# Kernel tuning notes

Hardware: AMD Instinct MI355X
Metric: run time of the kernel (lower is better)

## Reference

```python
import jax, jax.numpy as jnp
import numpy as np

D_MODEL = 1024
N_HEADS = 16
D_HEAD = D_MODEL // N_HEADS


def setup_inputs() -> dict:
    key = jax.random.key(0)
    k_x, k_wqkv, k_bqkv, k_wo, k_bo = jax.random.split(key, 5)
    B, S = 2, 2048
    x = jax.random.normal(k_x, (B, S, D_MODEL), dtype=jnp.float32)
    # torch Linear: y = x @ W.T + b; store W as [out, in] like torch
    bound1 = 1.0 / np.sqrt(D_MODEL)
    W_qkv = jax.random.uniform(k_wqkv, (3 * D_MODEL, D_MODEL), minval=-bound1, maxval=bound1, dtype=jnp.float32)
    b_qkv = jax.random.uniform(k_bqkv, (3 * D_MODEL,), minval=-bound1, maxval=bound1, dtype=jnp.float32)
    W_out = jax.random.uniform(k_wo, (D_MODEL, D_MODEL), minval=-bound1, maxval=bound1, dtype=jnp.float32)
    b_out = jax.random.uniform(k_bo, (D_MODEL,), minval=-bound1, maxval=bound1, dtype=jnp.float32)
    return {"x": x, "W_qkv": W_qkv, "b_qkv": b_qkv, "W_out": W_out, "b_out": b_out}


def reference(x, W_qkv, b_qkv, W_out, b_out):
    B, S, D = x.shape
    qkv = x @ W_qkv.T + b_qkv                       # [B, S, 3D]
    qkv = qkv.reshape(B, S, 3, N_HEADS, D_HEAD)
    qkv = jnp.transpose(qkv, (2, 0, 3, 1, 4))       # [3, B, H, S, Dh]
    q, k, v = qkv[0], qkv[1], qkv[2]
    scores = jnp.einsum('bhqd,bhkd->bhqk', q, k) / np.sqrt(D_HEAD).astype(np.float32)
    causal = jnp.tril(jnp.ones((S, S), dtype=bool))
    scores = jnp.where(causal[None, None], scores, jnp.float32(-jnp.inf))
    attn = jax.nn.softmax(scores, axis=-1)          # dropout p=0 -> identity
    out = jnp.einsum('bhqk,bhkd->bhqd', attn, v)    # [B, H, S, Dh]
    out = jnp.transpose(out, (0, 2, 1, 3)).reshape(B, S, D)
    return out @ W_out.T + b_out
```

## Files before the change

### kernel.cpp

```cpp
#include <hip/hip_runtime.h>
#include <hip/hip_bf16.h>
#include <cstdint>


#define DEV __device__ __forceinline__

#define VT_STRIDE 2048

using bf16x8 = __attribute__((ext_vector_type(8))) short;
using f32x4  = __attribute__((ext_vector_type(4))) float;

DEV unsigned short f2bf(float f) {
  unsigned u = __builtin_bit_cast(unsigned, f);
  u = (u + 0x7fffu + ((u >> 16) & 1u)) >> 16;
  return (unsigned short)u;
}

typedef __attribute__((address_space(1))) unsigned int as1_uint;
typedef __attribute__((address_space(3))) unsigned int as3_uint;

DEV void gload_lds16(const void* g, void* l) {
  __builtin_amdgcn_global_load_lds(
      (as1_uint*)(uintptr_t)g,
      (as3_uint*)(unsigned int)(uintptr_t)l,
      16, 0, 0);
}

#define N4_X  (4096 * 1024 / 4)
#define N4_WQ (3072 * 1024 / 4)
#define N4_WO (1024 * 1024 / 4)
__global__ __launch_bounds__(256) void cvt_all_k(const float* __restrict__ x,
                                                 const float* __restrict__ wq,
                                                 const float* __restrict__ wo,
                                                 unsigned short* __restrict__ xb,
                                                 unsigned short* __restrict__ wqb,
                                                 unsigned short* __restrict__ wob) {
  int i = blockIdx.x * 256 + threadIdx.x;
  const float* in; unsigned short* out;
  if (i < N4_X)                { in = x;  out = xb; }
  else if (i < N4_X + N4_WQ)   { i -= N4_X;  in = wq; out = wqb; }
  else                         { i -= N4_X + N4_WQ; in = wo; out = wob; }
  float4 v = reinterpret_cast<const float4*>(in)[i];
  ushort4 o;
  o.x = f2bf(v.x); o.y = f2bf(v.y); o.z = f2bf(v.z); o.w = f2bf(v.w);
  reinterpret_cast<ushort4*>(out)[i] = o;
}

__global__ __launch_bounds__(256) void transpose_v_k(const unsigned short* __restrict__ V,
                                                     unsigned short* __restrict__ Vt) {
  const int bh = blockIdx.x;
  const int st = blockIdx.y;
  const int tid = threadIdx.x;
  __shared__ unsigned short T[64 * 64];
  const unsigned short* src = V + ((size_t)bh * 2048 + st * 64) * 64;

#pragma unroll
  for (int it = 0; it < 2; ++it) {
    const int c = it * 256 + tid;
    const int L = c * 16;
    const int S = L ^ (((L >> 10) & 7) << 4);
    gload_lds16((const char*)src + S, (char*)T + L);
  }
  __syncthreads();

#pragma unroll
  for (int it = 0; it < 2; ++it) {
    const int c = it * 256 + tid;
    const int d = c >> 3;
    const int s_off = (c & 7) * 8;
    const int xg = (c & 7) << 4;
    bf16x8 pk;
#pragma unroll
    for (int j = 0; j < 8; ++j)
      pk[j] = *(const short*)((const char*)T + (((s_off + j) * 128 + d * 2) ^ xg));
    *(bf16x8*)(Vt + (size_t)(bh * 64 + d) * VT_STRIDE + st * 64 + s_off) = pk;
  }
}

template <int MODE, int N, int K>
__global__ __launch_bounds__(256) void gemm_bt(const unsigned short* __restrict__ A,
                                               const unsigned short* __restrict__ W,
                                               const float* __restrict__ bias,
                                               float* __restrict__ Cout,
                                               unsigned short* __restrict__ Qp,
                                               unsigned short* __restrict__ Kp,
                                               unsigned short* __restrict__ Vp) {
  __shared__ unsigned short As[128 * 64];
  __shared__ unsigned short Bs[128 * 64];
  const int tid = threadIdx.x;
  const int m0 = blockIdx.x * 128;
  const int n0 = blockIdx.y * 128;
  const int w = tid >> 6, lane = tid & 63, g = lane >> 4, lr = lane & 15;
  const int wr = w >> 1, wc = w & 1;
  const int xr = (lr & 7) << 4;

  f32x4 acc[4][4];
#pragma unroll
  for (int i = 0; i < 4; ++i)
#pragma unroll
    for (int j = 0; j < 4; ++j)
#pragma unroll
      for (int r = 0; r < 4; ++r) acc[i][j][r] = 0.f;

  for (int kt = 0; kt < K; kt += 64) {
#pragma unroll
    for (int it = 0; it < 4; ++it) {
      const int c = it * 256 + tid;
      const int row = c >> 3;
      const int colb = ((c & 7) * 16) ^ ((row & 7) << 4);
      gload_lds16((const char*)(A + (size_t)(m0 + row) * K + kt) + colb, (char*)As + c * 16);
      gload_lds16((const char*)(W + (size_t)(n0 + row) * K + kt) + colb, (char*)Bs + c * 16);
    }
    __syncthreads();
#pragma unroll
    for (int ks = 0; ks < 2; ++ks) {
      bf16x8 af[4], bf[4];
#pragma unroll
      for (int mi = 0; mi < 4; ++mi)
        af[mi] = *(const bf16x8*)((const char*)As +
                   ((((wr * 64 + mi * 16 + lr) * 128) + ks * 64 + g * 16) ^ xr));
#pragma unroll
      for (int ni = 0; ni < 4; ++ni)
        bf[ni] = *(const bf16x8*)((const char*)Bs +
                   ((((wc * 64 + ni * 16 + lr) * 128) + ks * 64 + g * 16) ^ xr));
#pragma unroll
      for (int mi = 0; mi < 4; ++mi)
#pragma unroll
        for (int ni = 0; ni < 4; ++ni)
          acc[mi][ni] = __builtin_amdgcn_mfma_f32_16x16x32_bf16(af[mi], bf[ni], acc[mi][ni], 0, 0, 0);
    }
    __syncthreads();
  }

  if (MODE == 0) {
#pragma unroll
    for (int ni = 0; ni < 4; ++ni) {
      const int col = n0 + wc * 64 + ni * 16 + lr;
      const float bv = bias[col];
#pragma unroll
      for (int mi = 0; mi < 4; ++mi)
#pragma unroll
        for (int r = 0; r < 4; ++r) {
          const int row = m0 + wr * 64 + mi * 16 + g * 4 + r;
          Cout[(size_t)row * N + col] = acc[mi][ni][r] + bv;
        }
    }
  } else {
#pragma unroll
    for (int ni = 0; ni < 4; ++ni) {
      const int col = n0 + wc * 64 + ni * 16 + lr;
      const float bv = bias[col];
      const int which = col >> 10;
      const int h = (col >> 6) & 15;
      const int d = col & 63;
      unsigned short* P = which == 0 ? Qp : which == 1 ? Kp : Vp;
#pragma unroll
      for (int mi = 0; mi < 4; ++mi)
#pragma unroll
        for (int r = 0; r < 4; ++r) {
          const int row = m0 + wr * 64 + mi * 16 + g * 4 + r;
          const int b = row >> 11, s = row & 2047;
          P[(((size_t)(b * 16 + h) * 2048 + s) << 6) + d] = f2bf(acc[mi][ni][r] + bv);
        }
    }
  }
}

__global__ __launch_bounds__(256) void attn_fwd(const unsigned short* __restrict__ Q,
                                                const unsigned short* __restrict__ Kg,
                                                const unsigned short* __restrict__ Vt,
                                                unsigned short* __restrict__ AO) {
  const int bh = blockIdx.x;
  const int qb = blockIdx.y;
  const int tid = threadIdx.x;
  const int w = tid >> 6, lane = tid & 63, g = lane >> 4, lr = lane & 15;
  const unsigned short* Qp = Q  + (size_t)bh * 2048 * 64;
  const unsigned short* Kp = Kg + (size_t)bh * 2048 * 64;
  const unsigned short* Vp = Vt + (size_t)bh * 64 * VT_STRIDE;
  const int b = bh >> 4, h = bh & 15;

  __shared__ unsigned short Ks[64 * 64];
  __shared__ unsigned short Vs[64 * 64];
  __shared__ unsigned short Pl[4][16 * 64];

  const float C = 0.1803368801f;
  char* Plw = (char*)Pl[w];
  const int xr = (lr & 7) << 4;

  const int L0 = tid * 16,         L1 = (tid + 256) * 16;
  const int G0 = L0 ^ (((L0 >> 7) & 7) << 4);
  const int G1 = L1 ^ (((L1 >> 7) & 7) << 4);

#pragma unroll
  for (int half = 0; half < 2; ++half) {
    const int qt = half ? (31 - qb) : qb;
    const int nb = qt + 1;
    const int qrow0 = qt * 64 + w * 16;

    bf16x8 aq[2];
#pragma unroll
    for (int ks = 0; ks < 2; ++ks)
      aq[ks] = *(const bf16x8*)(Qp + (size_t)(qrow0 + lr) * 64 + ks * 32 + g * 8);

    f32x4 o[4];
    float lp[4];
#pragma unroll
    for (int db = 0; db < 4; ++db)
#pragma unroll
      for (int r = 0; r < 4; ++r) o[db][r] = 0.f;
#pragma unroll
    for (int r = 0; r < 4; ++r) lp[r] = 0.f;

    for (int t = 0; t < nb; ++t) {
      const int kvb = t * 64;
      gload_lds16((const char*)Kp + (size_t)kvb * 128 + G0, (char*)Ks + L0);
      gload_lds16((const char*)Kp + (size_t)kvb * 128 + G1, (char*)Ks + L1);
      gload_lds16((const char*)Vp + (size_t)(G0 >> 7) * (VT_STRIDE * 2) + (size_t)kvb * 2 + (G0 & 127),
                  (char*)Vs + L0);
      gload_lds16((const char*)Vp + (size_t)(G1 >> 7) * (VT_STRIDE * 2) + (size_t)kvb * 2 + (G1 & 127),
                  (char*)Vs + L1);
      __syncthreads();

      f32x4 sc[4];
#pragma unroll
      for (int f = 0; f < 4; ++f)
#pragma unroll
        for (int r = 0; r < 4; ++r) sc[f][r] = 0.f;
#pragma unroll
      for (int ks = 0; ks < 2; ++ks)
#pragma unroll
        for (int f = 0; f < 4; ++f) {
          bf16x8 bk = *(const bf16x8*)((const char*)Ks + (((f * 16 + lr) * 128 + ks * 64 + g * 16) ^ xr));
          sc[f] = __builtin_amdgcn_mfma_f32_16x16x32_bf16(aq[ks], bk, sc[f], 0, 0, 0);
        }

      if (t == nb - 1) {
#pragma unroll
        for (int r = 0; r < 4; ++r) {
          const int qr = w * 16 + g * 4 + r;
#pragma unroll
          for (int f = 0; f < 4; ++f)
            if (f * 16 + lr > qr) sc[f][r] = -INFINITY;
        }
      }

#pragma unroll
      for (int r = 0; r < 4; ++r) {
        float s0 = exp2f(sc[0][r] * C);
        float s1 = exp2f(sc[1][r] * C);
        float s2 = exp2f(sc[2][r] * C);
        float s3 = exp2f(sc[3][r] * C);
        sc[0][r] = s0; sc[1][r] = s1; sc[2][r] = s2; sc[3][r] = s3;
        lp[r] += (s0 + s1) + (s2 + s3);
      }

#pragma unroll
      for (int r = 0; r < 4; ++r) {
        const int prow = g * 4 + r;
#pragma unroll
        for (int f = 0; f < 4; ++f) {
          const int byte = (prow * 128 + (f * 16 + lr) * 2) ^ ((prow & 7) << 4);
          *(unsigned short*)(Plw + byte) = f2bf(sc[f][r]);
        }
      }
      asm volatile("s_waitcnt lgkmcnt(0)" ::: "memory");
      __builtin_amdgcn_sched_barrier(0);

#pragma unroll
      for (int ks = 0; ks < 2; ++ks) {
        const int pbyte = (lr * 128 + ks * 64 + g * 16) ^ ((lr & 7) << 4);
        bf16x8 pa = *(const bf16x8*)(Plw + pbyte);
#pragma unroll
        for (int db = 0; db < 4; ++db) {
          bf16x8 bv = *(const bf16x8*)((const char*)Vs + (((db * 16 + lr) * 128 + ks * 64 + g * 16) ^ xr));
          o[db] = __builtin_amdgcn_mfma_f32_16x16x32_bf16(pa, bv, o[db], 0, 0, 0);
        }
      }
      __syncthreads();
    }

#pragma unroll
    for (int r = 0; r < 4; ++r) {
      float l = lp[r];
      l += __shfl_xor(l, 1); l += __shfl_xor(l, 2);
      l += __shfl_xor(l, 4); l += __shfl_xor(l, 8);
      lp[r] = 1.0f / l;
    }
#pragma unroll
    for (int r = 0; r < 4; ++r) {
      const int row = qrow0 + g * 4 + r;
#pragma unroll
      for (int db = 0; db < 4; ++db)
        AO[(size_t)(b * 2048 + row) * 1024 + h * 64 + db * 16 + lr] = f2bf(o[db][r] * lp[r]);
    }
  }
}

extern "C" void kernel_launch(void* const* d_in, const int* in_sizes, int n_in,
                              void* d_out, int out_size, void* d_ws, size_t ws_size,
                              hipStream_t stream) {
  const float* x     = (const float*)d_in[0];
  const float* W_qkv = (const float*)d_in[1];
  const float* b_qkv = (const float*)d_in[2];
  const float* W_out = (const float*)d_in[3];
  const float* b_out = (const float*)d_in[4];
  float* out = (float*)d_out;

  char* ws = (char*)d_ws;
  unsigned short* xb  = (unsigned short*)(ws);
  unsigned short* AOb = (unsigned short*)(ws);
  unsigned short* wqb = (unsigned short*)(ws + ((size_t)8 << 20));
  unsigned short* wob = (unsigned short*)(ws + ((size_t)14 << 20));
  unsigned short* Qb  = (unsigned short*)(ws + ((size_t)16 << 20));
  unsigned short* Kb  = (unsigned short*)(ws + ((size_t)24 << 20));
  unsigned short* Vb  = (unsigned short*)(ws + ((size_t)32 << 20));
  unsigned short* Vtb = (unsigned short*)(ws + ((size_t)40 << 20));

  cvt_all_k<<<(N4_X + N4_WQ + N4_WO) / 256, 256, 0, stream>>>(x, W_qkv, W_out, xb, wqb, wob);

  gemm_bt<1, 3072, 1024><<<dim3(32, 24), 256, 0, stream>>>(xb, wqb, b_qkv, nullptr, Qb, Kb, Vb);
  transpose_v_k<<<dim3(32, 32), 256, 0, stream>>>(Vb, Vtb);
  attn_fwd<<<dim3(32, 16), 256, 0, stream>>>(Qb, Kb, Vtb, AOb);
  gemm_bt<0, 1024, 1024><<<dim3(32, 8), 256, 0, stream>>>(AOb, wob, b_out, out, nullptr, nullptr, nullptr);
}
```

Measured before the change: 129.3 us.

## Double-buffer K/V tiles in attention and transpose QK^T MFMA layout

The attention kernel now keeps two LDS buffers for K and V and prefetches the next tile asynchronously while computing the current one, using partial vmcnt waits and raw barriers instead of a full syncthreads per iteration. The QK^T MFMA operands are swapped so each lane holds a score column, which lets P be packed with v_cvt_pk_bf16_f32 and written as 8-byte stores, and reduces the row-sum to two shuffles. s_setprio hints are added around the MFMA blocks. The cost is doubled LDS use for K/V, which may lower occupancy, plus more delicate synchronisation.

```diff
diff --git a/kernel.cpp b/kernel.cpp
--- a/kernel.cpp
+++ b/kernel.cpp
@@ -179,8 +179,8 @@
   const unsigned short* Vp = Vt + (size_t)bh * 64 * VT_STRIDE;
   const int b = bh >> 4, h = bh & 15;
 
-  __shared__ unsigned short Ks[64 * 64];
-  __shared__ unsigned short Vs[64 * 64];
+  __shared__ unsigned short Ks[2][64 * 64];
+  __shared__ unsigned short Vs[2][64 * 64];
   __shared__ unsigned short Pl[4][16 * 64];
 
   const float C = 0.1803368801f;
@@ -190,6 +190,16 @@
   const int L0 = tid * 16,         L1 = (tid + 256) * 16;
   const int G0 = L0 ^ (((L0 >> 7) & 7) << 4);
   const int G1 = L1 ^ (((L1 >> 7) & 7) << 4);
+
+#define STAGE(buf, kvb)                                                                     \
+  do {                                                                                      \
+    gload_lds16((const char*)Kp + (size_t)(kvb) * 128 + G0, (char*)Ks[buf] + L0);           \
+    gload_lds16((const char*)Kp + (size_t)(kvb) * 128 + G1, (char*)Ks[buf] + L1);           \
+    gload_lds16((const char*)Vp + (size_t)(G0 >> 7) * (VT_STRIDE * 2) + (size_t)(kvb) * 2 + \
+                    (G0 & 127), (char*)Vs[buf] + L0);                                       \
+    gload_lds16((const char*)Vp + (size_t)(G1 >> 7) * (VT_STRIDE * 2) + (size_t)(kvb) * 2 + \
+                    (G1 & 127), (char*)Vs[buf] + L1);                                       \
+  } while (0)
 
 #pragma unroll
   for (int half = 0; half < 2; ++half) {
@@ -203,97 +213,104 @@
       aq[ks] = *(const bf16x8*)(Qp + (size_t)(qrow0 + lr) * 64 + ks * 32 + g * 8);
 
     f32x4 o[4];
-    float lp[4];
+    float lp = 0.f;
 #pragma unroll
     for (int db = 0; db < 4; ++db)
 #pragma unroll
       for (int r = 0; r < 4; ++r) o[db][r] = 0.f;
-#pragma unroll
-    for (int r = 0; r < 4; ++r) lp[r] = 0.f;
+
+    STAGE(0, 0);
+    int cur = 0;
 
     for (int t = 0; t < nb; ++t) {
-      const int kvb = t * 64;
-      gload_lds16((const char*)Kp + (size_t)kvb * 128 + G0, (char*)Ks + L0);
-      gload_lds16((const char*)Kp + (size_t)kvb * 128 + G1, (char*)Ks + L1);
-      gload_lds16((const char*)Vp + (size_t)(G0 >> 7) * (VT_STRIDE * 2) + (size_t)kvb * 2 + (G0 & 127),
-                  (char*)Vs + L0);
-      gload_lds16((const char*)Vp + (size_t)(G1 >> 7) * (VT_STRIDE * 2) + (size_t)kvb * 2 + (G1 & 127),
-                  (char*)Vs + L1);
-      __syncthreads();
+      if (t + 1 < nb) {
+        STAGE(cur ^ 1, (t + 1) * 64);
+        asm volatile("s_waitcnt vmcnt(4)" ::: "memory");
+      } else {
+        asm volatile("s_waitcnt vmcnt(0)" ::: "memory");
+      }
+      __builtin_amdgcn_s_barrier();
+      __builtin_amdgcn_sched_barrier(0);
+
+      const char* KsC = (const char*)Ks[cur];
+      const char* VsC = (const char*)Vs[cur];
 
       f32x4 sc[4];
 #pragma unroll
       for (int f = 0; f < 4; ++f)
 #pragma unroll
         for (int r = 0; r < 4; ++r) sc[f][r] = 0.f;
+      __builtin_amdgcn_s_setprio(1);
 #pragma unroll
       for (int ks = 0; ks < 2; ++ks)
 #pragma unroll
         for (int f = 0; f < 4; ++f) {
-          bf16x8 bk = *(const bf16x8*)((const char*)Ks + (((f * 16 + lr) * 128 + ks * 64 + g * 16) ^ xr));
-          sc[f] = __builtin_amdgcn_mfma_f32_16x16x32_bf16(aq[ks], bk, sc[f], 0, 0, 0);
+          bf16x8 bk = *(const bf16x8*)(KsC + (((f * 16 + lr) * 128 + ks * 64 + g * 16) ^ xr));
+          sc[f] = __builtin_amdgcn_mfma_f32_16x16x32_bf16(bk, aq[ks], sc[f], 0, 0, 0);
         }
+      __builtin_amdgcn_s_setprio(0);
 
       if (t == nb - 1) {
-#pragma unroll
-        for (int r = 0; r < 4; ++r) {
-          const int qr = w * 16 + g * 4 + r;
-#pragma unroll
-          for (int f = 0; f < 4; ++f)
-            if (f * 16 + lr > qr) sc[f][r] = -INFINITY;
-        }
-      }
-
-#pragma unroll
-      for (int r = 0; r < 4; ++r) {
-        float s0 = exp2f(sc[0][r] * C);
-        float s1 = exp2f(sc[1][r] * C);
-        float s2 = exp2f(sc[2][r] * C);
-        float s3 = exp2f(sc[3][r] * C);
-        sc[0][r] = s0; sc[1][r] = s1; sc[2][r] = s2; sc[3][r] = s3;
-        lp[r] += (s0 + s1) + (s2 + s3);
-      }
-
-#pragma unroll
-      for (int r = 0; r < 4; ++r) {
-        const int prow = g * 4 + r;
-#pragma unroll
-        for (int f = 0; f < 4; ++f) {
-          const int byte = (prow * 128 + (f * 16 + lr) * 2) ^ ((prow & 7) << 4);
-          *(unsigned short*)(Plw + byte) = f2bf(sc[f][r]);
-        }
+        const int thr = w * 16 + lr - g * 4;
+#pragma unroll
+        for (int f = 0; f < 4; ++f)
+#pragma unroll
+          for (int r = 0; r < 4; ++r)
+            if (f * 16 + r > thr) sc[f][r] = -INFINITY;
+      }
+
+#pragma unroll
+      for (int f = 0; f < 4; ++f) {
+        float p0 = exp2f(sc[f][0] * C);
+        float p1 = exp2f(sc[f][1] * C);
+        float p2 = exp2f(sc[f][2] * C);
+        float p3 = exp2f(sc[f][3] * C);
+        sc[f][0] = p0; sc[f][1] = p1; sc[f][2] = p2; sc[f][3] = p3;
+        lp += (p0 + p1) + (p2 + p3);
+      }
+
+#pragma unroll
+      for (int f = 0; f < 4; ++f) {
+        unsigned w0, w1;
+        asm("v_cvt_pk_bf16_f32 %0, %1, %2" : "=v"(w0) : "v"(sc[f][0]), "v"(sc[f][1]));
+        asm("v_cvt_pk_bf16_f32 %0, %1, %2" : "=v"(w1) : "v"(sc[f][2]), "v"(sc[f][3]));
+        uint2 pk; pk.x = w0; pk.y = w1;
+        *(uint2*)(Plw + ((lr * 128 + f * 32 + g * 8) ^ xr)) = pk;
       }
       asm volatile("s_waitcnt lgkmcnt(0)" ::: "memory");
       __builtin_amdgcn_sched_barrier(0);
 
+      __builtin_amdgcn_s_setprio(1);
 #pragma unroll
       for (int ks = 0; ks < 2; ++ks) {
-        const int pbyte = (lr * 128 + ks * 64 + g * 16) ^ ((lr & 7) << 4);
-        bf16x8 pa = *(const bf16x8*)(Plw + pbyte);
+        bf16x8 pa = *(const bf16x8*)(Plw + ((lr * 128 + ks * 64 + g * 16) ^ xr));
 #pragma unroll
         for (int db = 0; db < 4; ++db) {
-          bf16x8 bv = *(const bf16x8*)((const char*)Vs + (((db * 16 + lr) * 128 + ks * 64 + g * 16) ^ xr));
+          bf16x8 bv = *(const bf16x8*)(VsC + (((db * 16 + lr) * 128 + ks * 64 + g * 16) ^ xr));
           o[db] = __builtin_amdgcn_mfma_f32_16x16x32_bf16(pa, bv, o[db], 0, 0, 0);
         }
       }
-      __syncthreads();
-    }
-
+      __builtin_amdgcn_s_setprio(0);
+
+      asm volatile("" ::: "memory");
+      __builtin_amdgcn_s_barrier();
+      __builtin_amdgcn_sched_barrier(0);
+      cur ^= 1;
+    }
+
+    lp += __shfl_xor(lp, 16);
+    lp += __shfl_xor(lp, 32);
+    const float inv = 1.0f / lp;
 #pragma unroll
     for (int r = 0; r < 4; ++r) {
-      float l = lp[r];
-      l += __shfl_xor(l, 1); l += __shfl_xor(l, 2);
-      l += __shfl_xor(l, 4); l += __shfl_xor(l, 8);
-      lp[r] = 1.0f / l;
-    }
-#pragma unroll
-    for (int r = 0; r < 4; ++r) {
+      const float linv = __shfl(inv, g * 4 + r);
       const int row = qrow0 + g * 4 + r;
 #pragma unroll
       for (int db = 0; db < 4; ++db)
-        AO[(size_t)(b * 2048 + row) * 1024 + h * 64 + db * 16 + lr] = f2bf(o[db][r] * lp[r]);
-    }
-  }
+        AO[(size_t)(b * 2048 + row) * 1024 + h * 64 + db * 16 + lr] = f2bf(o[db][r] * linv);
+    }
+  }
+#undef STAGE
 }
 
 extern "C" void kernel_launch(void* const* d_in, const int* in_sizes, int n_in,
```

Measured after the change: 124.0 us. 4.1% less time.
